# Optimization experiments

Hardware: AMD Instinct MI355X
Metric: run time of the kernel (lower is better)

Reference implementation:

```python
import jax, jax.numpy as jnp
import numpy as np

D_K = 64

def setup_inputs() -> dict:
    key = jax.random.key(0)
    ks = jax.random.split(key, 9)
    B, S, D = 8, 2048, 512
    d_k, d_v = 64, 64
    return {
        "q_in": jax.random.normal(ks[0], (B, S, D), jnp.float32),
        "k_in": jax.random.normal(ks[1], (B, S, D), jnp.float32),
        "v_in": jax.random.normal(ks[2], (B, S, D), jnp.float32),
        "Wq": jax.random.normal(ks[3], (D, d_k), jnp.float32) * 0.05,
        "bq": jax.random.normal(ks[4], (d_k,), jnp.float32) * 0.05,
        "Wk": jax.random.normal(ks[5], (D, d_k), jnp.float32) * 0.05,
        "bk": jax.random.normal(ks[6], (d_k,), jnp.float32) * 0.05,
        "Wv": jax.random.normal(ks[7], (D, d_v), jnp.float32) * 0.05,
        "bv": jax.random.normal(ks[8], (d_v,), jnp.float32) * 0.05,
    }

def reference(q_in, k_in, v_in, Wq, bq, Wk, bk, Wv, bv):
    # Dense projections: x @ W + b
    q = jnp.einsum('bsd,dk->bsk', q_in, Wq) + bq  # [B,S,d_k]
    k = jnp.einsum('bsd,dk->bsk', k_in, Wk) + bk  # [B,S,d_k]
    v = jnp.einsum('bsd,dv->bsv', v_in, Wv) + bv  # [B,S,d_v]
    scale = 1.0 / np.sqrt(D_K).astype(np.float32)
    scores = jnp.einsum('bqk,bsk->bqs', q, k) * scale  # [B,S,S]
    attn = jax.nn.softmax(scores, axis=-1)
    return jnp.einsum('bqs,bsv->bqv', attn, v)  # [B,S,d_v]
```

## Files before the change

kernel.cpp:

```cpp
#include <hip/hip_runtime.h>
#include <hip/hip_bf16.h>
#include <cstdint>

typedef __attribute__((ext_vector_type(8))) short short8;
typedef __attribute__((ext_vector_type(16))) float f32x16;

#if __has_builtin(__builtin_amdgcn_exp2f)
#define EXP2F(x) __builtin_amdgcn_exp2f(x)
#else
#define EXP2F(x) exp2f(x)
#endif

#define MFMA32(A, B, C) __builtin_amdgcn_mfma_f32_32x32x16_bf16((A), (B), (C), 0, 0, 0)

__device__ __forceinline__ unsigned short f2bf(float f) {
  unsigned int u = __builtin_bit_cast(unsigned int, f);
  u += 0x7FFFu + ((u >> 16) & 1u);
  return (unsigned short)(u >> 16);
}

__global__ __launch_bounds__(256) void prep_wt(
    const float* __restrict__ Wq, const float* __restrict__ Wk,
    const float* __restrict__ Wv, unsigned short* __restrict__ Wt)
{
  int idx = blockIdx.x * 256 + threadIdx.x;
  int which = idx >> 15;
  int rem = idx & 32767;
  int n = rem >> 9;
  int k = rem & 511;
  const float* W = (which == 0) ? Wq : (which == 1) ? Wk : Wv;
  Wt[idx] = f2bf(W[k * 64 + n]);
}

__global__ __launch_bounds__(256, 3) void proj_kernel(
    const float* __restrict__ qin, const float* __restrict__ kin,
    const float* __restrict__ vin, const unsigned short* __restrict__ Wt,
    const float* __restrict__ bq, const float* __restrict__ bk,
    const float* __restrict__ bv,
    unsigned short* __restrict__ Qo, unsigned short* __restrict__ Ko,
    unsigned short* __restrict__ Vto)
{
  __shared__ unsigned short Xs[2][64 * 136];

  const int which = blockIdx.y;
  const float* X    = (which == 0) ? qin : (which == 1) ? kin : vin;
  const float* bias = (which == 0) ? bq  : (which == 1) ? bk  : bv;

  const int tid = threadIdx.x;
  const int lane = tid & 63, wv = tid >> 6;
  const int h = lane >> 5, l31 = lane & 31;
  const int grp = wv & 1, nh = wv >> 1;
  const int m0 = blockIdx.x * 64;

  const unsigned short* wcol =
      Wt + (size_t)which * 64 * 512 + (size_t)(nh * 32 + l31) * 512 + h * 8;

  const int srow = tid >> 5;
  const int skoff = tid & 31;
  const float* xg = X + (size_t)(m0 + srow) * 512 + skoff * 4;

  float4 ld[8];
  #pragma unroll
  for (int j = 0; j < 8; ++j)
    ld[j] = *(const float4*)(xg + (size_t)(8 * j) * 512);
  #pragma unroll
  for (int j = 0; j < 8; ++j) {
    unsigned int w0 = (unsigned int)f2bf(ld[j].x) | ((unsigned int)f2bf(ld[j].y) << 16);
    unsigned int w1 = (unsigned int)f2bf(ld[j].z) | ((unsigned int)f2bf(ld[j].w) << 16);
    uint2 pw; pw.x = w0; pw.y = w1;
    *(uint2*)(&Xs[0][(srow + 8 * j) * 136 + skoff * 4]) = pw;
  }
  __syncthreads();

  f32x16 acc = {};
  for (int c = 0; c < 4; ++c) {
    if (c < 3) {
      #pragma unroll
      for (int j = 0; j < 8; ++j)
        ld[j] = *(const float4*)(xg + (size_t)(8 * j) * 512 + (c + 1) * 128);
    }
    const unsigned short* arow = &Xs[c & 1][(grp * 32 + l31) * 136 + h * 8];
    const unsigned short* wk = wcol + c * 128;
    #pragma unroll
    for (int ks = 0; ks < 8; ++ks) {
      short8 af = *(const short8*)(arow + ks * 16);
      short8 bf = *(const short8*)(wk + ks * 16);
      acc = MFMA32(af, bf, acc);
    }
    if (c < 3) {
      #pragma unroll
      for (int j = 0; j < 8; ++j) {
        unsigned int w0 = (unsigned int)f2bf(ld[j].x) | ((unsigned int)f2bf(ld[j].y) << 16);
        unsigned int w1 = (unsigned int)f2bf(ld[j].z) | ((unsigned int)f2bf(ld[j].w) << 16);
        uint2 pw; pw.x = w0; pw.y = w1;
        *(uint2*)(&Xs[(c + 1) & 1][(srow + 8 * j) * 136 + skoff * 4]) = pw;
      }
      __syncthreads();
    }
  }

  const float bv0 = bias[nh * 32 + l31];

  if (which < 2) {
    const float scale = which ? 1.0f : 0.18033688f;
    unsigned short* Y = which ? Ko : Qo;
    #pragma unroll
    for (int r = 0; r < 16; ++r) {
      int row = (r & 3) + 8 * (r >> 2) + 4 * h;
      Y[(size_t)(m0 + grp * 32 + row) * 64 + nh * 32 + l31] =
          f2bf((acc[r] + bv0) * scale);
    }
  } else {
    __syncthreads();
    unsigned short* TB = &Xs[0][0];
    #pragma unroll
    for (int r = 0; r < 16; ++r) {
      int row = (r & 3) + 8 * (r >> 2) + 4 * h;
      TB[(nh * 32 + l31) * 68 + grp * 32 + row] = f2bf(acc[r] + bv0);
    }
    __syncthreads();
    int bidx = blockIdx.x >> 5;
    int s0 = (blockIdx.x & 31) * 64;
    for (int i = tid; i < 64 * 16; i += 256) {
      int n = i >> 4, cs = i & 15;
      ushort4 v4 = *(const ushort4*)(TB + n * 68 + cs * 4);
      *(ushort4*)(Vto + ((size_t)bidx * 64 + n) * 2048 + s0 + cs * 4) = v4;
    }
  }
}

__global__ __launch_bounds__(512, 2) void attn_kernel(
    const unsigned short* __restrict__ Q, const unsigned short* __restrict__ K,
    const unsigned short* __restrict__ Vt, float* __restrict__ out)
{
  __shared__ float ObS[4][16][64];
  __shared__ float MpS[4][64];
  __shared__ float LpS[4][64];

  const int tid = threadIdx.x;
  const int lane = tid & 63, w = tid >> 6;
  const int h = lane >> 5, l31 = lane & 31;
  const int b = blockIdx.y;
  const int q0 = blockIdx.x * 64;

  short8 qf[2][4];
  #pragma unroll
  for (int qt = 0; qt < 2; ++qt) {
    const unsigned short* qp = Q + ((size_t)(b * 2048 + q0 + qt * 32 + l31)) * 64 + h * 8;
    #pragma unroll
    for (int c = 0; c < 4; ++c) qf[qt][c] = *(const short8*)(qp + c * 16);
  }

  f32x16 o00 = {}, o01 = {}, o10 = {}, o11 = {};
  float m0 = -1e30f, m1 = -1e30f, ls0 = 0.f, ls1 = 0.f;

  const unsigned short* Kp  = K  + ((size_t)(b * 2048 + w * 256 + l31)) * 64 + h * 8;
  const unsigned short* Vp0 = Vt + ((size_t)(b * 64 + l31)) * 2048 + w * 256 + h * 8;
  const unsigned short* Vp1 = Vp0 + (size_t)32 * 2048;

  short8 kf[4], vf0[2], vf1[2];
  #pragma unroll
  for (int c = 0; c < 4; ++c) kf[c] = *(const short8*)(Kp + c * 16);
  vf0[0] = *(const short8*)(Vp0); vf0[1] = *(const short8*)(Vp0 + 16);
  vf1[0] = *(const short8*)(Vp1); vf1[1] = *(const short8*)(Vp1 + 16);

  auto process = [&](f32x16 sT, float &m, float &ls, f32x16 &oA, f32x16 &oB) {
    float tm[8];
    #pragma unroll
    for (int i = 0; i < 8; ++i) tm[i] = fmaxf(sT[2 * i], sT[2 * i + 1]);
    #pragma unroll
    for (int i = 0; i < 4; ++i) tm[i] = fmaxf(tm[i], tm[i + 4]);
    float mx = fmaxf(fmaxf(tm[0], tm[1]), fmaxf(tm[2], tm[3]));
    mx = fmaxf(mx, __shfl_xor(mx, 32, 64));
    if (__any(mx > m + 8.0f)) {
      float mnew = fmaxf(m, mx);
      float alpha = EXP2F(m - mnew);
      m = mnew;
      ls *= alpha; oA *= alpha; oB *= alpha;
    }
    float p[16];
    #pragma unroll
    for (int r = 0; r < 16; ++r) p[r] = EXP2F(sT[r] - m);
    float ts[8];
    #pragma unroll
    for (int i = 0; i < 8; ++i) ts[i] = p[2 * i] + p[2 * i + 1];
    #pragma unroll
    for (int i = 0; i < 4; ++i) ts[i] += ts[i + 4];
    float rs = (ts[0] + ts[1]) + (ts[2] + ts[3]);
    rs += __shfl_xor(rs, 32, 64);
    ls += rs;
    unsigned int pk[8];
    #pragma unroll
    for (int i = 0; i < 8; ++i)
      pk[i] = (unsigned int)f2bf(p[2 * i]) | ((unsigned int)f2bf(p[2 * i + 1]) << 16);
    unsigned int ex[8];
    #pragma unroll
    for (int i = 0; i < 8; ++i) ex[i] = (unsigned int)__shfl_xor((int)pk[i], 32, 64);
    uint4 cc0, cc1;
    if (h == 0) { cc0 = make_uint4(pk[0], pk[1], ex[0], ex[1]); cc1 = make_uint4(pk[4], pk[5], ex[4], ex[5]); }
    else        { cc0 = make_uint4(ex[2], ex[3], pk[2], pk[3]); cc1 = make_uint4(ex[6], ex[7], pk[6], pk[7]); }
    short8 P0 = __builtin_bit_cast(short8, cc0);
    short8 P1 = __builtin_bit_cast(short8, cc1);
    __builtin_amdgcn_s_setprio(1);
    oA = MFMA32(vf0[0], P0, oA); oA = MFMA32(vf0[1], P1, oA);
    oB = MFMA32(vf1[0], P0, oB); oB = MFMA32(vf1[1], P1, oB);
    __builtin_amdgcn_s_setprio(0);
  };

  for (int st = 0; st < 8; ++st) {
    f32x16 s0 = {}, s1 = {};
    __builtin_amdgcn_s_setprio(1);
    #pragma unroll
    for (int c = 0; c < 4; ++c) s0 = MFMA32(kf[c], qf[0][c], s0);
    #pragma unroll
    for (int c = 0; c < 4; ++c) s1 = MFMA32(kf[c], qf[1][c], s1);
    __builtin_amdgcn_s_setprio(0);
    if (st < 7) {
      #pragma unroll
      for (int c = 0; c < 4; ++c)
        kf[c] = *(const short8*)(Kp + (size_t)(st + 1) * 2048 + c * 16);
    }
    process(s0, m0, ls0, o00, o10);
    process(s1, m1, ls1, o01, o11);
    if (st < 7) {
      vf0[0] = *(const short8*)(Vp0 + (st + 1) * 32);
      vf0[1] = *(const short8*)(Vp0 + (st + 1) * 32 + 16);
      vf1[0] = *(const short8*)(Vp1 + (st + 1) * 32);
      vf1[1] = *(const short8*)(Vp1 + (st + 1) * 32 + 16);
    }
  }

  for (int half = 4; half > 0; half >>= 1) {
    const bool writer = (w >= half) && (w < 2 * half);
    const bool merger = (w < half);
    __syncthreads();
    if (writer && h == 0) {
      MpS[w - half][l31] = m0;      LpS[w - half][l31] = ls0;
      MpS[w - half][32 + l31] = m1; LpS[w - half][32 + l31] = ls1;
    }
    __syncthreads();
    float fb0 = 0.f, fb1 = 0.f;
    if (merger) {
      float pm0 = MpS[w][l31],      pl0 = LpS[w][l31];
      float pm1 = MpS[w][32 + l31], pl1 = LpS[w][32 + l31];
      float nm0 = fmaxf(m0, pm0), nm1 = fmaxf(m1, pm1);
      float fa0 = EXP2F(m0 - nm0); fb0 = EXP2F(pm0 - nm0);
      float fa1 = EXP2F(m1 - nm1); fb1 = EXP2F(pm1 - nm1);
      m0 = nm0; m1 = nm1;
      ls0 = ls0 * fa0 + pl0 * fb0; ls1 = ls1 * fa1 + pl1 * fb1;
      o00 *= fa0; o10 *= fa0; o01 *= fa1; o11 *= fa1;
    }
    __syncthreads();
    if (writer) {
      #pragma unroll
      for (int r = 0; r < 16; ++r) ObS[w - half][r][lane] = o00[r]; }
    __syncthreads();
    if (merger) {
      #pragma unroll
      for (int r = 0; r < 16; ++r) o00[r] += ObS[w][r][lane] * fb0; }
    __syncthreads();
    if (writer) {
      #pragma unroll
      for (int r = 0; r < 16; ++r) ObS[w - half][r][lane] = o01[r]; }
    __syncthreads();
    if (merger) {
      #pragma unroll
      for (int r = 0; r < 16; ++r) o01[r] += ObS[w][r][lane] * fb1; }
    __syncthreads();
    if (writer) {
      #pragma unroll
      for (int r = 0; r < 16; ++r) ObS[w - half][r][lane] = o10[r]; }
    __syncthreads();
    if (merger) {
      #pragma unroll
      for (int r = 0; r < 16; ++r) o10[r] += ObS[w][r][lane] * fb0; }
    __syncthreads();
    if (writer) {
      #pragma unroll
      for (int r = 0; r < 16; ++r) ObS[w - half][r][lane] = o11[r]; }
    __syncthreads();
    if (merger) {
      #pragma unroll
      for (int r = 0; r < 16; ++r) o11[r] += ObS[w][r][lane] * fb1; }
  }

  if (w == 0) {
    float i0 = 1.0f / ls0, i1 = 1.0f / ls1;
    o00 *= i0; o10 *= i0; o01 *= i1; o11 *= i1;
    #pragma unroll
    for (int qt = 0; qt < 2; ++qt) {
      int q = qt * 32 + l31;
      float* ob = out + ((size_t)(b * 2048 + q0 + q)) * 64 + 4 * h;
      const f32x16 a = qt ? o01 : o00;
      const f32x16 c = qt ? o11 : o10;
      #pragma unroll
      for (int g = 0; g < 4; ++g) {
        *(float4*)(ob + 8 * g)      = make_float4(a[4*g], a[4*g+1], a[4*g+2], a[4*g+3]);
        *(float4*)(ob + 32 + 8 * g) = make_float4(c[4*g], c[4*g+1], c[4*g+2], c[4*g+3]);
      }
    }
  }
}

extern "C" void kernel_launch(void* const* d_in, const int* in_sizes, int n_in,
                              void* d_out, int out_size, void* d_ws, size_t ws_size,
                              hipStream_t stream) {
  const float* qin = (const float*)d_in[0];
  const float* kin = (const float*)d_in[1];
  const float* vin = (const float*)d_in[2];
  const float* Wq  = (const float*)d_in[3];
  const float* bq  = (const float*)d_in[4];
  const float* Wk  = (const float*)d_in[5];
  const float* bk  = (const float*)d_in[6];
  const float* Wv  = (const float*)d_in[7];
  const float* bv  = (const float*)d_in[8];

  unsigned short* Qo  = (unsigned short*)d_ws;
  unsigned short* Ko  = Qo + (size_t)16384 * 64;
  unsigned short* Vto = Ko + (size_t)16384 * 64;
  unsigned short* Wt  = Vto + (size_t)8 * 64 * 2048;
  float* out = (float*)d_out;

  hipLaunchKernelGGL(prep_wt, dim3(384), dim3(256), 0, stream, Wq, Wk, Wv, Wt);
  hipLaunchKernelGGL(proj_kernel, dim3(256, 3), dim3(256), 0, stream,
                     qin, kin, vin, Wt, bq, bk, bv, Qo, Ko, Vto);
  hipLaunchKernelGGL(attn_kernel, dim3(32, 8), dim3(512), 0, stream, Qo, Ko, Vto, out);
}
```

Before: 161.4 us.

## Fuse weight conversion into projection and halve attention query tile per block

Drops the separate prep_wt kernel. The projection kernel now reads fp32 weights directly, converts them to bf16 in registers and double-buffers them across K chunks, which saves one launch and a workspace round trip but makes the weight reads strided. The attention kernel now handles 32 queries per block instead of 64, with 512 blocks and launch bounds raised to 4 blocks per CU. This is meant to raise occupancy and cut register pressure, at the cost of loading K and V twice as often per query.

```diff
diff --git a/kernel.cpp b/kernel.cpp
--- a/kernel.cpp
+++ b/kernel.cpp
@@ -19,22 +19,11 @@
   return (unsigned short)(u >> 16);
 }
 
-__global__ __launch_bounds__(256) void prep_wt(
-    const float* __restrict__ Wq, const float* __restrict__ Wk,
-    const float* __restrict__ Wv, unsigned short* __restrict__ Wt)
-{
-  int idx = blockIdx.x * 256 + threadIdx.x;
-  int which = idx >> 15;
-  int rem = idx & 32767;
-  int n = rem >> 9;
-  int k = rem & 511;
-  const float* W = (which == 0) ? Wq : (which == 1) ? Wk : Wv;
-  Wt[idx] = f2bf(W[k * 64 + n]);
-}
-
 __global__ __launch_bounds__(256, 3) void proj_kernel(
     const float* __restrict__ qin, const float* __restrict__ kin,
-    const float* __restrict__ vin, const unsigned short* __restrict__ Wt,
+    const float* __restrict__ vin,
+    const float* __restrict__ Wq, const float* __restrict__ Wk,
+    const float* __restrict__ Wv,
     const float* __restrict__ bq, const float* __restrict__ bk,
     const float* __restrict__ bv,
     unsigned short* __restrict__ Qo, unsigned short* __restrict__ Ko,
@@ -44,6 +33,7 @@
 
   const int which = blockIdx.y;
   const float* X    = (which == 0) ? qin : (which == 1) ? kin : vin;
+  const float* W    = (which == 0) ? Wq  : (which == 1) ? Wk  : Wv;
   const float* bias = (which == 0) ? bq  : (which == 1) ? bk  : bv;
 
   const int tid = threadIdx.x;
@@ -52,12 +42,29 @@
   const int grp = wv & 1, nh = wv >> 1;
   const int m0 = blockIdx.x * 64;
 
-  const unsigned short* wcol =
-      Wt + (size_t)which * 64 * 512 + (size_t)(nh * 32 + l31) * 512 + h * 8;
+  const float* Wn = W + nh * 32 + l31;
 
   const int srow = tid >> 5;
   const int skoff = tid & 31;
   const float* xg = X + (size_t)(m0 + srow) * 512 + skoff * 4;
+
+  short8 wfA[8], wfB[8];
+  auto loadW = [&](short8 (&dst)[8], int c) {
+    #pragma unroll
+    for (int ks = 0; ks < 8; ++ks) {
+      const float* wp = Wn + (size_t)(c * 128 + ks * 16 + h * 8) * 64;
+      float w0 = wp[0*64], w1 = wp[1*64], w2 = wp[2*64], w3 = wp[3*64];
+      float w4 = wp[4*64], w5 = wp[5*64], w6 = wp[6*64], w7 = wp[7*64];
+      uint4 uu;
+      uu.x = (unsigned int)f2bf(w0) | ((unsigned int)f2bf(w1) << 16);
+      uu.y = (unsigned int)f2bf(w2) | ((unsigned int)f2bf(w3) << 16);
+      uu.z = (unsigned int)f2bf(w4) | ((unsigned int)f2bf(w5) << 16);
+      uu.w = (unsigned int)f2bf(w6) | ((unsigned int)f2bf(w7) << 16);
+      dst[ks] = __builtin_bit_cast(short8, uu);
+    }
+  };
+
+  loadW(wfA, 0);
 
   float4 ld[8];
   #pragma unroll
@@ -73,19 +80,20 @@
   __syncthreads();
 
   f32x16 acc = {};
+  #pragma unroll
   for (int c = 0; c < 4; ++c) {
     if (c < 3) {
       #pragma unroll
       for (int j = 0; j < 8; ++j)
         ld[j] = *(const float4*)(xg + (size_t)(8 * j) * 512 + (c + 1) * 128);
+      if (c & 1) loadW(wfA, c + 1); else loadW(wfB, c + 1);
     }
     const unsigned short* arow = &Xs[c & 1][(grp * 32 + l31) * 136 + h * 8];
-    const unsigned short* wk = wcol + c * 128;
+    const short8 (&wfC)[8] = (c & 1) ? wfB : wfA;
     #pragma unroll
     for (int ks = 0; ks < 8; ++ks) {
       short8 af = *(const short8*)(arow + ks * 16);
-      short8 bf = *(const short8*)(wk + ks * 16);
-      acc = MFMA32(af, bf, acc);
+      acc = MFMA32(af, wfC[ks], acc);
     }
     if (c < 3) {
       #pragma unroll
@@ -129,30 +137,29 @@
   }
 }
 
-__global__ __launch_bounds__(512, 2) void attn_kernel(
+__global__ __launch_bounds__(512, 4) void attn_kernel(
     const unsigned short* __restrict__ Q, const unsigned short* __restrict__ K,
     const unsigned short* __restrict__ Vt, float* __restrict__ out)
 {
   __shared__ float ObS[4][16][64];
-  __shared__ float MpS[4][64];
-  __shared__ float LpS[4][64];
+  __shared__ float MpS[4][32];
+  __shared__ float LpS[4][32];
 
   const int tid = threadIdx.x;
   const int lane = tid & 63, w = tid >> 6;
   const int h = lane >> 5, l31 = lane & 31;
   const int b = blockIdx.y;
-  const int q0 = blockIdx.x * 64;
-
-  short8 qf[2][4];
-  #pragma unroll
-  for (int qt = 0; qt < 2; ++qt) {
-    const unsigned short* qp = Q + ((size_t)(b * 2048 + q0 + qt * 32 + l31)) * 64 + h * 8;
-    #pragma unroll
-    for (int c = 0; c < 4; ++c) qf[qt][c] = *(const short8*)(qp + c * 16);
-  }
-
-  f32x16 o00 = {}, o01 = {}, o10 = {}, o11 = {};
-  float m0 = -1e30f, m1 = -1e30f, ls0 = 0.f, ls1 = 0.f;
+  const int q0 = blockIdx.x * 32;
+
+  short8 qf[4];
+  {
+    const unsigned short* qp = Q + ((size_t)(b * 2048 + q0 + l31)) * 64 + h * 8;
+    #pragma unroll
+    for (int c = 0; c < 4; ++c) qf[c] = *(const short8*)(qp + c * 16);
+  }
+
+  f32x16 o00 = {}, o10 = {};
+  float m0 = -1e30f, ls0 = 0.f;
 
   const unsigned short* Kp  = K  + ((size_t)(b * 2048 + w * 256 + l31)) * 64 + h * 8;
   const unsigned short* Vp0 = Vt + ((size_t)(b * 64 + l31)) * 2048 + w * 256 + h * 8;
@@ -164,7 +171,17 @@
   vf0[0] = *(const short8*)(Vp0); vf0[1] = *(const short8*)(Vp0 + 16);
   vf1[0] = *(const short8*)(Vp1); vf1[1] = *(const short8*)(Vp1 + 16);
 
-  auto process = [&](f32x16 sT, float &m, float &ls, f32x16 &oA, f32x16 &oB) {
+  for (int st = 0; st < 8; ++st) {
+    f32x16 sT = {};
+    __builtin_amdgcn_s_setprio(1);
+    #pragma unroll
+    for (int c = 0; c < 4; ++c) sT = MFMA32(kf[c], qf[c], sT);
+    __builtin_amdgcn_s_setprio(0);
+    if (st < 7) {
+      #pragma unroll
+      for (int c = 0; c < 4; ++c)
+        kf[c] = *(const short8*)(Kp + (size_t)(st + 1) * 2048 + c * 16);
+    }
     float tm[8];
     #pragma unroll
     for (int i = 0; i < 8; ++i) tm[i] = fmaxf(sT[2 * i], sT[2 * i + 1]);
@@ -172,15 +189,15 @@
     for (int i = 0; i < 4; ++i) tm[i] = fmaxf(tm[i], tm[i + 4]);
     float mx = fmaxf(fmaxf(tm[0], tm[1]), fmaxf(tm[2], tm[3]));
     mx = fmaxf(mx, __shfl_xor(mx, 32, 64));
-    if (__any(mx > m + 8.0f)) {
-      float mnew = fmaxf(m, mx);
-      float alpha = EXP2F(m - mnew);
-      m = mnew;
-      ls *= alpha; oA *= alpha; oB *= alpha;
+    if (__any(mx > m0 + 8.0f)) {
+      float mnew = fmaxf(m0, mx);
+      float alpha = EXP2F(m0 - mnew);
+      m0 = mnew;
+      ls0 *= alpha; o00 *= alpha; o10 *= alpha;
     }
     float p[16];
     #pragma unroll
-    for (int r = 0; r < 16; ++r) p[r] = EXP2F(sT[r] - m);
+    for (int r = 0; r < 16; ++r) p[r] = EXP2F(sT[r] - m0);
     float ts[8];
     #pragma unroll
     for (int i = 0; i < 8; ++i) ts[i] = p[2 * i] + p[2 * i + 1];
@@ -188,7 +205,7 @@
     for (int i = 0; i < 4; ++i) ts[i] += ts[i + 4];
     float rs = (ts[0] + ts[1]) + (ts[2] + ts[3]);
     rs += __shfl_xor(rs, 32, 64);
-    ls += rs;
+    ls0 += rs;
     unsigned int pk[8];
     #pragma unroll
     for (int i = 0; i < 8; ++i)
@@ -202,26 +219,9 @@
     short8 P0 = __builtin_bit_cast(short8, cc0);
     short8 P1 = __builtin_bit_cast(short8, cc1);
     __builtin_amdgcn_s_setprio(1);
-    oA = MFMA32(vf0[0], P0, oA); oA = MFMA32(vf0[1], P1, oA);
-    oB = MFMA32(vf1[0], P0, oB); oB = MFMA32(vf1[1], P1, oB);
+    o00 = MFMA32(vf0[0], P0, o00); o00 = MFMA32(vf0[1], P1, o00);
+    o10 = MFMA32(vf1[0], P0, o10); o10 = MFMA32(vf1[1], P1, o10);
     __builtin_amdgcn_s_setprio(0);
-  };
-
-  for (int st = 0; st < 8; ++st) {
-    f32x16 s0 = {}, s1 = {};
-    __builtin_amdgcn_s_setprio(1);
-    #pragma unroll
-    for (int c = 0; c < 4; ++c) s0 = MFMA32(kf[c], qf[0][c], s0);
-    #pragma unroll
-    for (int c = 0; c < 4; ++c) s1 = MFMA32(kf[c], qf[1][c], s1);
-    __builtin_amdgcn_s_setprio(0);
-    if (st < 7) {
-      #pragma unroll
-      for (int c = 0; c < 4; ++c)
-        kf[c] = *(const short8*)(Kp + (size_t)(st + 1) * 2048 + c * 16);
-    }
-    process(s0, m0, ls0, o00, o10);
-    process(s1, m1, ls1, o01, o11);
     if (st < 7) {
       vf0[0] = *(const short8*)(Vp0 + (st + 1) * 32);
       vf0[1] = *(const short8*)(Vp0 + (st + 1) * 32 + 16);
@@ -235,20 +235,17 @@
     const bool merger = (w < half);
     __syncthreads();
     if (writer && h == 0) {
-      MpS[w - half][l31] = m0;      LpS[w - half][l31] = ls0;
-      MpS[w - half][32 + l31] = m1; LpS[w - half][32 + l31] = ls1;
-    }
-    __syncthreads();
-    float fb0 = 0.f, fb1 = 0.f;
+      MpS[w - half][l31] = m0; LpS[w - half][l31] = ls0;
+    }
+    __syncthreads();
+    float fb0 = 0.f;
     if (merger) {
-      float pm0 = MpS[w][l31],      pl0 = LpS[w][l31];
-      float pm1 = MpS[w][32 + l31], pl1 = LpS[w][32 + l31];
-      float nm0 = fmaxf(m0, pm0), nm1 = fmaxf(m1, pm1);
+      float pm0 = MpS[w][l31], pl0 = LpS[w][l31];
+      float nm0 = fmaxf(m0, pm0);
       float fa0 = EXP2F(m0 - nm0); fb0 = EXP2F(pm0 - nm0);
-      float fa1 = EXP2F(m1 - nm1); fb1 = EXP2F(pm1 - nm1);
-      m0 = nm0; m1 = nm1;
-      ls0 = ls0 * fa0 + pl0 * fb0; ls1 = ls1 * fa1 + pl1 * fb1;
-      o00 *= fa0; o10 *= fa0; o01 *= fa1; o11 *= fa1;
+      m0 = nm0;
+      ls0 = ls0 * fa0 + pl0 * fb0;
+      o00 *= fa0; o10 *= fa0;
     }
     __syncthreads();
     if (writer) {
@@ -261,43 +258,21 @@
     __syncthreads();
     if (writer) {
       #pragma unroll
-      for (int r = 0; r < 16; ++r) ObS[w - half][r][lane] = o01[r]; }
+      for (int r = 0; r < 16; ++r) ObS[w - half][r][lane] = o10[r]; }
     __syncthreads();
     if (merger) {
       #pragma unroll
-      for (int r = 0; r < 16; ++r) o01[r] += ObS[w][r][lane] * fb1; }
-    __syncthreads();
-    if (writer) {
-      #pragma unroll
-      for (int r = 0; r < 16; ++r) ObS[w - half][r][lane] = o10[r]; }
-    __syncthreads();
-    if (merger) {
-      #pragma unroll
       for (int r = 0; r < 16; ++r) o10[r] += ObS[w][r][lane] * fb0; }
-    __syncthreads();
-    if (writer) {
-      #pragma unroll
-      for (int r = 0; r < 16; ++r) ObS[w - half][r][lane] = o11[r]; }
-    __syncthreads();
-    if (merger) {
-      #pragma unroll
-      for (int r = 0; r < 16; ++r) o11[r] += ObS[w][r][lane] * fb1; }
   }
 
   if (w == 0) {
-    float i0 = 1.0f / ls0, i1 = 1.0f / ls1;
-    o00 *= i0; o10 *= i0; o01 *= i1; o11 *= i1;
-    #pragma unroll
-    for (int qt = 0; qt < 2; ++qt) {
-      int q = qt * 32 + l31;
-      float* ob = out + ((size_t)(b * 2048 + q0 + q)) * 64 + 4 * h;
-      const f32x16 a = qt ? o01 : o00;
-      const f32x16 c = qt ? o11 : o10;
-      #pragma unroll
-      for (int g = 0; g < 4; ++g) {
-        *(float4*)(ob + 8 * g)      = make_float4(a[4*g], a[4*g+1], a[4*g+2], a[4*g+3]);
-        *(float4*)(ob + 32 + 8 * g) = make_float4(c[4*g], c[4*g+1], c[4*g+2], c[4*g+3]);
-      }
+    float i0 = 1.0f / ls0;
+    o00 *= i0; o10 *= i0;
+    float* ob = out + ((size_t)(b * 2048 + q0 + l31)) * 64 + 4 * h;
+    #pragma unroll
+    for (int g = 0; g < 4; ++g) {
+      *(float4*)(ob + 8 * g)      = make_float4(o00[4*g], o00[4*g+1], o00[4*g+2], o00[4*g+3]);
+      *(float4*)(ob + 32 + 8 * g) = make_float4(o10[4*g], o10[4*g+1], o10[4*g+2], o10[4*g+3]);
     }
   }
 }
@@ -318,11 +293,9 @@
   unsigned short* Qo  = (unsigned short*)d_ws;
   unsigned short* Ko  = Qo + (size_t)16384 * 64;
   unsigned short* Vto = Ko + (size_t)16384 * 64;
-  unsigned short* Wt  = Vto + (size_t)8 * 64 * 2048;
   float* out = (float*)d_out;
 
-  hipLaunchKernelGGL(prep_wt, dim3(384), dim3(256), 0, stream, Wq, Wk, Wv, Wt);
   hipLaunchKernelGGL(proj_kernel, dim3(256, 3), dim3(256), 0, stream,
-                     qin, kin, vin, Wt, bq, bk, bv, Qo, Ko, Vto);
-  hipLaunchKernelGGL(attn_kernel, dim3(32, 8), dim3(512), 0, stream, Qo, Ko, Vto, out);
+                     qin, kin, vin, Wq, Wk, Wv, bq, bk, bv, Qo, Ko, Vto);
+  hipLaunchKernelGGL(attn_kernel, dim3(64, 8), dim3(512), 0, stream, Qo, Ko, Vto, out);
 }
```

Result: slower. 188.0 us (+16.5%).

## Load projection A operands directly from global, dropping LDS staging

Applied to the files above, without the earlier changes.

The projection kernel drops the shared-memory double buffer and syncthreads. Each wave now loads its fp32 input rows straight from global into registers, converts them to bf16 fragments in flight, and computes both 32-column halves with two accumulators through a 4-deep register prefetch ring. The V transpose writes go directly from registers as ushort4 stores instead of through LDS. This removes LDS traffic and barriers, but global reads become per-lane 32-byte strided accesses that coalesce less well, and register pressure rises.

```diff
diff --git a/kernel.cpp b/kernel.cpp
--- a/kernel.cpp
+++ b/kernel.cpp
@@ -17,6 +17,15 @@
   unsigned int u = __builtin_bit_cast(unsigned int, f);
   u += 0x7FFFu + ((u >> 16) & 1u);
   return (unsigned short)(u >> 16);
+}
+
+__device__ __forceinline__ short8 packA(const float4 &a0, const float4 &a1) {
+  uint4 uu;
+  uu.x = (unsigned int)f2bf(a0.x) | ((unsigned int)f2bf(a0.y) << 16);
+  uu.y = (unsigned int)f2bf(a0.z) | ((unsigned int)f2bf(a0.w) << 16);
+  uu.z = (unsigned int)f2bf(a1.x) | ((unsigned int)f2bf(a1.y) << 16);
+  uu.w = (unsigned int)f2bf(a1.z) | ((unsigned int)f2bf(a1.w) << 16);
+  return __builtin_bit_cast(short8, uu);
 }
 
 __global__ __launch_bounds__(256) void prep_wt(
@@ -32,7 +41,20 @@
   Wt[idx] = f2bf(W[k * 64 + n]);
 }
 
-__global__ __launch_bounds__(256, 3) void proj_kernel(
+#define PJ_LOAD(S, ks) do { \
+    a##S##0 = *(const float4*)(ap + (size_t)(ks) * 16); \
+    a##S##1 = *(const float4*)(ap + (size_t)(ks) * 16 + 4); \
+    b##S##0 = *(const short8*)(bp0 + (ks) * 16); \
+    b##S##1 = *(const short8*)(bp1 + (ks) * 16); \
+  } while (0)
+
+#define PJ_STEP(S) do { \
+    short8 af = packA(a##S##0, a##S##1); \
+    acc0 = MFMA32(af, b##S##0, acc0); \
+    acc1 = MFMA32(af, b##S##1, acc1); \
+  } while (0)
+
+__global__ __launch_bounds__(128) void proj_kernel(
     const float* __restrict__ qin, const float* __restrict__ kin,
     const float* __restrict__ vin, const unsigned short* __restrict__ Wt,
     const float* __restrict__ bq, const float* __restrict__ bk,
@@ -40,66 +62,35 @@
     unsigned short* __restrict__ Qo, unsigned short* __restrict__ Ko,
     unsigned short* __restrict__ Vto)
 {
-  __shared__ unsigned short Xs[2][64 * 136];
-
   const int which = blockIdx.y;
   const float* X    = (which == 0) ? qin : (which == 1) ? kin : vin;
   const float* bias = (which == 0) ? bq  : (which == 1) ? bk  : bv;
 
   const int tid = threadIdx.x;
-  const int lane = tid & 63, wv = tid >> 6;
+  const int lane = tid & 63, w = tid >> 6;
   const int h = lane >> 5, l31 = lane & 31;
-  const int grp = wv & 1, nh = wv >> 1;
-  const int m0 = blockIdx.x * 64;
-
-  const unsigned short* wcol =
-      Wt + (size_t)which * 64 * 512 + (size_t)(nh * 32 + l31) * 512 + h * 8;
-
-  const int srow = tid >> 5;
-  const int skoff = tid & 31;
-  const float* xg = X + (size_t)(m0 + srow) * 512 + skoff * 4;
-
-  float4 ld[8];
-  #pragma unroll
-  for (int j = 0; j < 8; ++j)
-    ld[j] = *(const float4*)(xg + (size_t)(8 * j) * 512);
-  #pragma unroll
-  for (int j = 0; j < 8; ++j) {
-    unsigned int w0 = (unsigned int)f2bf(ld[j].x) | ((unsigned int)f2bf(ld[j].y) << 16);
-    unsigned int w1 = (unsigned int)f2bf(ld[j].z) | ((unsigned int)f2bf(ld[j].w) << 16);
-    uint2 pw; pw.x = w0; pw.y = w1;
-    *(uint2*)(&Xs[0][(srow + 8 * j) * 136 + skoff * 4]) = pw;
-  }
-  __syncthreads();
-
-  f32x16 acc = {};
-  for (int c = 0; c < 4; ++c) {
-    if (c < 3) {
-      #pragma unroll
-      for (int j = 0; j < 8; ++j)
-        ld[j] = *(const float4*)(xg + (size_t)(8 * j) * 512 + (c + 1) * 128);
-    }
-    const unsigned short* arow = &Xs[c & 1][(grp * 32 + l31) * 136 + h * 8];
-    const unsigned short* wk = wcol + c * 128;
-    #pragma unroll
-    for (int ks = 0; ks < 8; ++ks) {
-      short8 af = *(const short8*)(arow + ks * 16);
-      short8 bf = *(const short8*)(wk + ks * 16);
-      acc = MFMA32(af, bf, acc);
-    }
-    if (c < 3) {
-      #pragma unroll
-      for (int j = 0; j < 8; ++j) {
-        unsigned int w0 = (unsigned int)f2bf(ld[j].x) | ((unsigned int)f2bf(ld[j].y) << 16);
-        unsigned int w1 = (unsigned int)f2bf(ld[j].z) | ((unsigned int)f2bf(ld[j].w) << 16);
-        uint2 pw; pw.x = w0; pw.y = w1;
-        *(uint2*)(&Xs[(c + 1) & 1][(srow + 8 * j) * 136 + skoff * 4]) = pw;
-      }
-      __syncthreads();
-    }
-  }
-
-  const float bv0 = bias[nh * 32 + l31];
+  const int m0 = (blockIdx.x * 2 + w) * 32;
+
+  const float* ap = X + (size_t)(m0 + l31) * 512 + h * 8;
+  const unsigned short* bp0 = Wt + (size_t)which * 32768 + (size_t)l31 * 512 + h * 8;
+  const unsigned short* bp1 = bp0 + 32 * 512;
+
+  f32x16 acc0 = {}, acc1 = {};
+
+  float4 a00, a01, a10, a11, a20, a21, a30, a31;
+  short8 b00, b01, b10, b11, b20, b21, b30, b31;
+
+  PJ_LOAD(0, 0); PJ_LOAD(1, 1); PJ_LOAD(2, 2); PJ_LOAD(3, 3);
+
+  for (int ks = 0; ks < 32; ks += 4) {
+    PJ_STEP(0); if (ks + 4 < 32) PJ_LOAD(0, ks + 4);
+    PJ_STEP(1); if (ks + 5 < 32) PJ_LOAD(1, ks + 5);
+    PJ_STEP(2); if (ks + 6 < 32) PJ_LOAD(2, ks + 6);
+    PJ_STEP(3); if (ks + 7 < 32) PJ_LOAD(3, ks + 7);
+  }
+
+  const float bi0 = bias[l31];
+  const float bi1 = bias[32 + l31];
 
   if (which < 2) {
     const float scale = which ? 1.0f : 0.18033688f;
@@ -107,24 +98,22 @@
     #pragma unroll
     for (int r = 0; r < 16; ++r) {
       int row = (r & 3) + 8 * (r >> 2) + 4 * h;
-      Y[(size_t)(m0 + grp * 32 + row) * 64 + nh * 32 + l31] =
-          f2bf((acc[r] + bv0) * scale);
+      Y[(size_t)(m0 + row) * 64 + l31]      = f2bf((acc0[r] + bi0) * scale);
+      Y[(size_t)(m0 + row) * 64 + 32 + l31] = f2bf((acc1[r] + bi1) * scale);
     }
   } else {
-    __syncthreads();
-    unsigned short* TB = &Xs[0][0];
-    #pragma unroll
-    for (int r = 0; r < 16; ++r) {
-      int row = (r & 3) + 8 * (r >> 2) + 4 * h;
-      TB[(nh * 32 + l31) * 68 + grp * 32 + row] = f2bf(acc[r] + bv0);
-    }
-    __syncthreads();
-    int bidx = blockIdx.x >> 5;
-    int s0 = (blockIdx.x & 31) * 64;
-    for (int i = tid; i < 64 * 16; i += 256) {
-      int n = i >> 4, cs = i & 15;
-      ushort4 v4 = *(const ushort4*)(TB + n * 68 + cs * 4);
-      *(ushort4*)(Vto + ((size_t)bidx * 64 + n) * 2048 + s0 + cs * 4) = v4;
+    const int bb = m0 >> 11;
+    const int s0 = m0 & 2047;
+    #pragma unroll
+    for (int g = 0; g < 4; ++g) {
+      const int s = s0 + 8 * g + 4 * h;
+      ushort4 v0, v1;
+      v0.x = f2bf(acc0[4 * g + 0] + bi0); v0.y = f2bf(acc0[4 * g + 1] + bi0);
+      v0.z = f2bf(acc0[4 * g + 2] + bi0); v0.w = f2bf(acc0[4 * g + 3] + bi0);
+      v1.x = f2bf(acc1[4 * g + 0] + bi1); v1.y = f2bf(acc1[4 * g + 1] + bi1);
+      v1.z = f2bf(acc1[4 * g + 2] + bi1); v1.w = f2bf(acc1[4 * g + 3] + bi1);
+      *(ushort4*)(Vto + ((size_t)(bb * 64 + l31)) * 2048 + s)      = v0;
+      *(ushort4*)(Vto + ((size_t)(bb * 64 + 32 + l31)) * 2048 + s) = v1;
     }
   }
 }
@@ -322,7 +311,7 @@
   float* out = (float*)d_out;
 
   hipLaunchKernelGGL(prep_wt, dim3(384), dim3(256), 0, stream, Wq, Wk, Wv, Wt);
-  hipLaunchKernelGGL(proj_kernel, dim3(256, 3), dim3(256), 0, stream,
+  hipLaunchKernelGGL(proj_kernel, dim3(256, 3), dim3(128), 0, stream,
                      qin, kin, vin, Wt, bq, bk, bv, Qo, Ko, Vto);
   hipLaunchKernelGGL(attn_kernel, dim3(32, 8), dim3(512), 0, stream, Qo, Ko, Vto, out);
 }
```

Result: slower. 178.7 us (+10.8%).

## Stage projection inputs via direct global-to-LDS loads with XOR swizzle

Applied to the files above, without the earlier changes.

The projection kernel now copies fp32 input tiles straight into shared memory with global_load_lds (bypassing registers), using an XOR-swizzled layout and double buffering over 8 chunks of 64 columns. The bf16 conversion moves to after the LDS read, right before each MFMA. This is meant to cut register pressure and the VGPR round trip of the old load-convert-store staging, and to overlap the next chunk's load with compute. In exchange it doubles the LDS footprint (fp32 instead of bf16), repeats the conversion per wave, adds more barriers, and drops the occupancy hint from launch bounds.

```diff
diff --git a/kernel.cpp b/kernel.cpp
--- a/kernel.cpp
+++ b/kernel.cpp
@@ -17,6 +17,15 @@
   unsigned int u = __builtin_bit_cast(unsigned int, f);
   u += 0x7FFFu + ((u >> 16) & 1u);
   return (unsigned short)(u >> 16);
+}
+
+__device__ __forceinline__ short8 packA(const float4 &a0, const float4 &a1) {
+  uint4 uu;
+  uu.x = (unsigned int)f2bf(a0.x) | ((unsigned int)f2bf(a0.y) << 16);
+  uu.y = (unsigned int)f2bf(a0.z) | ((unsigned int)f2bf(a0.w) << 16);
+  uu.z = (unsigned int)f2bf(a1.x) | ((unsigned int)f2bf(a1.y) << 16);
+  uu.w = (unsigned int)f2bf(a1.z) | ((unsigned int)f2bf(a1.w) << 16);
+  return __builtin_bit_cast(short8, uu);
 }
 
 __global__ __launch_bounds__(256) void prep_wt(
@@ -32,7 +41,7 @@
   Wt[idx] = f2bf(W[k * 64 + n]);
 }
 
-__global__ __launch_bounds__(256, 3) void proj_kernel(
+__global__ __launch_bounds__(256) void proj_kernel(
     const float* __restrict__ qin, const float* __restrict__ kin,
     const float* __restrict__ vin, const unsigned short* __restrict__ Wt,
     const float* __restrict__ bq, const float* __restrict__ bk,
@@ -40,7 +49,7 @@
     unsigned short* __restrict__ Qo, unsigned short* __restrict__ Ko,
     unsigned short* __restrict__ Vto)
 {
-  __shared__ unsigned short Xs[2][64 * 136];
+  __shared__ float Xf[2][64 * 64];
 
   const int which = blockIdx.y;
   const float* X    = (which == 0) ? qin : (which == 1) ? kin : vin;
@@ -53,50 +62,47 @@
   const int m0 = blockIdx.x * 64;
 
   const unsigned short* wcol =
-      Wt + (size_t)which * 64 * 512 + (size_t)(nh * 32 + l31) * 512 + h * 8;
-
-  const int srow = tid >> 5;
-  const int skoff = tid & 31;
-  const float* xg = X + (size_t)(m0 + srow) * 512 + skoff * 4;
-
-  float4 ld[8];
+      Wt + (size_t)which * 32768 + (size_t)(nh * 32 + l31) * 512 + h * 8;
+
+  const int srow4 = tid >> 4;
+  const int sslot = tid & 15;
+
+  auto stage = [&](int chunk, int buf) {
+    #pragma unroll
+    for (int k = 0; k < 4; ++k) {
+      const int row = k * 16 + srow4;
+      const int l = sslot ^ (row & 15);
+      const float* gp = X + (size_t)(m0 + row) * 512 + chunk * 64 + l * 4;
+      char* lp = (char*)&Xf[buf][0] + k * 4096 + wv * 1024;
+      __builtin_amdgcn_global_load_lds(
+          (const __attribute__((address_space(1))) unsigned int*)gp,
+          (__attribute__((address_space(3))) unsigned int*)lp, 16, 0, 0);
+    }
+  };
+
+  stage(0, 0);
+  __syncthreads();
+
+  f32x16 acc = {};
+  int buf = 0;
   #pragma unroll
-  for (int j = 0; j < 8; ++j)
-    ld[j] = *(const float4*)(xg + (size_t)(8 * j) * 512);
-  #pragma unroll
-  for (int j = 0; j < 8; ++j) {
-    unsigned int w0 = (unsigned int)f2bf(ld[j].x) | ((unsigned int)f2bf(ld[j].y) << 16);
-    unsigned int w1 = (unsigned int)f2bf(ld[j].z) | ((unsigned int)f2bf(ld[j].w) << 16);
-    uint2 pw; pw.x = w0; pw.y = w1;
-    *(uint2*)(&Xs[0][(srow + 8 * j) * 136 + skoff * 4]) = pw;
-  }
-  __syncthreads();
-
-  f32x16 acc = {};
-  for (int c = 0; c < 4; ++c) {
-    if (c < 3) {
-      #pragma unroll
-      for (int j = 0; j < 8; ++j)
-        ld[j] = *(const float4*)(xg + (size_t)(8 * j) * 512 + (c + 1) * 128);
-    }
-    const unsigned short* arow = &Xs[c & 1][(grp * 32 + l31) * 136 + h * 8];
-    const unsigned short* wk = wcol + c * 128;
-    #pragma unroll
-    for (int ks = 0; ks < 8; ++ks) {
-      short8 af = *(const short8*)(arow + ks * 16);
+  for (int c = 0; c < 8; ++c) {
+    if (c < 7) stage(c + 1, buf ^ 1);
+    const int r = grp * 32 + l31;
+    const float* arow = &Xf[buf][r * 64];
+    const int rx = r & 15;
+    const unsigned short* wk = wcol + c * 64;
+    #pragma unroll
+    for (int ks = 0; ks < 4; ++ks) {
+      const int s0 = ks * 4 + h * 2;
+      float4 x0 = *(const float4*)(arow + ((s0 ^ rx) * 4));
+      float4 x1 = *(const float4*)(arow + (((s0 + 1) ^ rx) * 4));
+      short8 af = packA(x0, x1);
       short8 bf = *(const short8*)(wk + ks * 16);
       acc = MFMA32(af, bf, acc);
     }
-    if (c < 3) {
-      #pragma unroll
-      for (int j = 0; j < 8; ++j) {
-        unsigned int w0 = (unsigned int)f2bf(ld[j].x) | ((unsigned int)f2bf(ld[j].y) << 16);
-        unsigned int w1 = (unsigned int)f2bf(ld[j].z) | ((unsigned int)f2bf(ld[j].w) << 16);
-        uint2 pw; pw.x = w0; pw.y = w1;
-        *(uint2*)(&Xs[(c + 1) & 1][(srow + 8 * j) * 136 + skoff * 4]) = pw;
-      }
-      __syncthreads();
-    }
+    __syncthreads();
+    buf ^= 1;
   }
 
   const float bv0 = bias[nh * 32 + l31];
@@ -112,7 +118,7 @@
     }
   } else {
     __syncthreads();
-    unsigned short* TB = &Xs[0][0];
+    unsigned short* TB = (unsigned short*)&Xf[0][0];
     #pragma unroll
     for (int r = 0; r < 16; ++r) {
       int row = (r & 3) + 8 * (r >> 2) + 4 * h;
```

Result: no change. 163.8 us (+1.5%).
